# Performance work log

Measured on AMD Instinct MI355X. Metric: run time of the kernel, lower is better.

The kernel has to match this reference:

```python
import jax, jax.numpy as jnp
import numpy as np

NUM_EMBEDDINGS = 8192
EMBEDDING_DIM = 64
COMMITMENT_COST = 0.25


def setup_inputs() -> dict:
    key = jax.random.key(0)
    kx, ke = jax.random.split(key)
    x = jax.random.normal(kx, (32, 1024, EMBEDDING_DIM), dtype=jnp.float32)
    embeddings = jax.random.normal(ke, (NUM_EMBEDDINGS, EMBEDDING_DIM), dtype=jnp.float32)
    return {"x": x, "embeddings": embeddings}


def reference(x, embeddings):
    d = embeddings.shape[1]
    flat_x = x.reshape(-1, d)  # [N, D]
    # squared euclidean distances (argmin identical to cdist argmin):
    d2 = (
        jnp.sum(flat_x * flat_x, axis=-1, keepdims=True)
        - 2.0 * flat_x @ embeddings.T
        + jnp.sum(embeddings * embeddings, axis=-1)
    )
    encoding_indices = jnp.argmin(d2, axis=1)  # [N]
    quantized = embeddings[encoding_indices].reshape(x.shape)
    codebook_loss = jnp.mean((jax.lax.stop_gradient(quantized) - x) ** 2)
    commitment_loss = COMMITMENT_COST * jnp.mean((quantized - jax.lax.stop_gradient(x)) ** 2)
    loss = codebook_loss + commitment_loss
    # straight-through estimator
    quantized_st = x + jax.lax.stop_gradient(quantized - x)
    return quantized_st, loss, encoding_indices
```

## Files before the change

### kernel.cpp

```cpp
#include <hip/hip_runtime.h>
#include <hip/hip_bf16.h>
#include <float.h>

#define N_ROWS 32768
#define DIMS   64
#define K_EMB  8192
#define NT     (K_EMB / 16)
#define NQ     8
#define NTQ    (NT / NQ)
#define TSTAGE 4
#define NSTAGE (NTQ / TSTAGE)
#define RG     4
#define KEYMASK 0xFFFFFFC0u
#define GAP_THR 3.5e-3f

typedef __attribute__((ext_vector_type(8))) short s8v;
typedef __attribute__((ext_vector_type(4))) float f4v;
typedef __attribute__((ext_vector_type(4))) int   i4v;

#define WS_EFRAG 0
#define WS_EN2   (2 * 1024 * 1024)
#define WS_IDX   (WS_EN2 + K_EMB * 4)
#define WS_KEY   (WS_IDX + N_ROWS * 4)
#define WS_BH    (WS_KEY + N_ROWS * 8)
#define WS_SH    (WS_BH + NQ * N_ROWS * 4)
#define WS_CH    (WS_SH + NQ * N_ROWS * 4)
#define WS_CTL   (WS_CH + NQ * N_ROWS * 4)
#define WS_WL    (WS_CTL + 16)

#define OUT_LOSS (N_ROWS * DIMS)
#define OUT_IDX  (N_ROWS * DIMS + 1)

__device__ inline short bfh(float v) {
    __hip_bfloat16 h = __float2bfloat16(v);
    return __builtin_bit_cast(short, h);
}
__device__ inline float bff(short s) {
    __hip_bfloat16 h = __builtin_bit_cast(__hip_bfloat16, s);
    return __bfloat162float(h);
}

__global__ void vq_prep(const float* __restrict__ emb, short* __restrict__ efrag,
                        float* __restrict__ en2, int4* __restrict__ ctl) {
    if (blockIdx.x == 0 && threadIdx.x == 0) *ctl = make_int4(0, 0, 0, 0);
    int gid = blockIdx.x * 256 + threadIdx.x;
    int t = gid >> 6, lane = gid & 63;
    int m = lane & 15, q = lane >> 4;
    const float* er = emb + (size_t)(t * 16 + m) * DIMS;
    s8v hi0, lo0, hi1, lo1;
    float ss = 0.f;
#pragma unroll
    for (int j = 0; j < 8; ++j) {
        float v0 = er[q * 8 + j];
        float v1 = er[32 + q * 8 + j];
        ss += v0 * v0 + v1 * v1;
        short h0 = bfh(v0); lo0[j] = bfh(v0 - bff(h0)); hi0[j] = h0;
        short h1 = bfh(v1); lo1[j] = bfh(v1 - bff(h1)); hi1[j] = h1;
    }
    s8v* base = (s8v*)efrag + (size_t)t * 4 * 64;
    base[0 * 64 + lane] = hi0;
    base[1 * 64 + lane] = hi1;
    base[2 * 64 + lane] = lo0;
    base[3 * 64 + lane] = lo1;
    ss += __shfl_xor(ss, 16, 64);
    ss += __shfl_xor(ss, 32, 64);
    if (q == 0) en2[t * 16 + m] = -0.5f * ss;
}

__global__ __launch_bounds__(256)
__attribute__((amdgpu_waves_per_eu(2, 4))) void vq_phase1(
    const float* __restrict__ x, const short* __restrict__ efrag,
    const float* __restrict__ en2,
    float* __restrict__ bh, float* __restrict__ sh, int* __restrict__ ch) {
    __shared__ __align__(16) char lds[2][TSTAGE * 4096];
    int tid = threadIdx.x, wid = tid >> 6, lane = tid & 63;
    int m = lane & 15, q = lane >> 4;
    int kh = blockIdx.y;
    int row0 = blockIdx.x * 256 + wid * 64;

    s8v ahi[RG][2], alo[RG][2];
#pragma unroll
    for (int g = 0; g < RG; ++g) {
        const float* xr = x + (size_t)(row0 + g * 16 + m) * DIMS + q * 8;
#pragma unroll
        for (int j = 0; j < 8; ++j) {
            float v0 = xr[j], v1 = xr[32 + j];
            short h0 = bfh(v0); alo[g][0][j] = bfh(v0 - bff(h0)); ahi[g][0][j] = h0;
            short h1 = bfh(v1); alo[g][1][j] = bfh(v1 - bff(h1)); ahi[g][1][j] = h1;
        }
    }

    float best[RG][4], sec[RG][4];
#pragma unroll
    for (int g = 0; g < RG; ++g)
#pragma unroll
        for (int r = 0; r < 4; ++r) { best[g][r] = -FLT_MAX; sec[g][r] = -FLT_MAX; }

    const char* gsrc = (const char*)efrag + (size_t)kh * NTQ * 4096;

#pragma unroll
    for (int i = 0; i < TSTAGE; ++i)
        __builtin_amdgcn_global_load_lds(
            (const __attribute__((address_space(1))) void*)(gsrc + i * 4096 + tid * 16),
            (__attribute__((address_space(3))) void*)(&lds[0][i * 4096 + tid * 16]),
            16, 0, 0);
    __syncthreads();

    for (int s = 0; s < NSTAGE; ++s) {
        int pb = s & 1;
        if (s + 1 < NSTAGE) {
            const char* gn = gsrc + (size_t)(s + 1) * TSTAGE * 4096;
#pragma unroll
            for (int i = 0; i < TSTAGE; ++i)
                __builtin_amdgcn_global_load_lds(
                    (const __attribute__((address_space(1))) void*)(gn + i * 4096 + tid * 16),
                    (__attribute__((address_space(3))) void*)(&lds[pb ^ 1][i * 4096 + tid * 16]),
                    16, 0, 0);
        }
        const i4v* B = (const i4v*)(lds[pb]);
        const float* ep = en2 + (size_t)(kh * NTQ + s * TSTAGE) * 16 + m;
#pragma unroll
        for (int tt = 0; tt < TSTAGE; ++tt) {
            i4v b0 = B[tt * 256 + 0 * 64 + lane];
            i4v b1 = B[tt * 256 + 1 * 64 + lane];
            i4v b2 = B[tt * 256 + 2 * 64 + lane];
            i4v b3 = B[tt * 256 + 3 * 64 + lane];
            float c0 = ep[tt * 16];
            unsigned code = (unsigned)(s * TSTAGE + tt);
            f4v cinit = {c0, c0, c0, c0};
#pragma unroll
            for (int g = 0; g < RG; ++g) {
                f4v acc;
                acc = __builtin_amdgcn_mfma_f32_16x16x32_bf16(ahi[g][0], __builtin_bit_cast(s8v, b0), cinit, 0, 0, 0);
                acc = __builtin_amdgcn_mfma_f32_16x16x32_bf16(ahi[g][1], __builtin_bit_cast(s8v, b1), acc, 0, 0, 0);
                acc = __builtin_amdgcn_mfma_f32_16x16x32_bf16(ahi[g][0], __builtin_bit_cast(s8v, b2), acc, 0, 0, 0);
                acc = __builtin_amdgcn_mfma_f32_16x16x32_bf16(ahi[g][1], __builtin_bit_cast(s8v, b3), acc, 0, 0, 0);
                acc = __builtin_amdgcn_mfma_f32_16x16x32_bf16(alo[g][0], __builtin_bit_cast(s8v, b0), acc, 0, 0, 0);
                acc = __builtin_amdgcn_mfma_f32_16x16x32_bf16(alo[g][1], __builtin_bit_cast(s8v, b1), acc, 0, 0, 0);
#pragma unroll
                for (int r = 0; r < 4; ++r) {
                    float kf = __uint_as_float(
                        (__float_as_uint(acc[r]) & KEYMASK) | code);
                    sec[g][r]  = __builtin_amdgcn_fmed3f(kf, sec[g][r], best[g][r]);
                    best[g][r] = fmaxf(best[g][r], kf);
                }
            }
        }
        __syncthreads();
    }

#pragma unroll
    for (int g = 0; g < RG; ++g)
#pragma unroll
    for (int r = 0; r < 4; ++r) {
        float b = best[g][r], sv = sec[g][r];
#pragma unroll
        for (int off = 1; off < 16; off <<= 1) {
            float ob = __shfl_xor(b, off, 64);
            float os = __shfl_xor(sv, off, 64);
            sv = fmaxf(fminf(b, ob), fmaxf(sv, os));
            b  = fmaxf(b, ob);
        }
        unsigned long long bal =
            __ballot(__float_as_uint(best[g][r]) == __float_as_uint(b));
        int win = __ffsll(bal >> (q * 16)) - 1;
        if (m == win) {
            int tl  = (int)(__float_as_uint(b) & 63u);
            int col = ((kh * NTQ + tl) << 4) | m;
            int o = kh * N_ROWS + row0 + g * 16 + q * 4 + r;
            bh[o] = b; sh[o] = sv; ch[o] = col;
        }
    }
}

__global__ void vq_merge(const float* __restrict__ bh, const float* __restrict__ sh,
                         const int* __restrict__ ch, int* __restrict__ idx_buf,
                         unsigned long long* __restrict__ key8,
                         float* __restrict__ nbv,
                         int* __restrict__ wl, int* __restrict__ wl_count) {
    int row = blockIdx.x * 256 + threadIdx.x;
    float nb = bh[row];
    int   c  = ch[row];
    float ns = -FLT_MAX;
#pragma unroll
    for (int h = 1; h < NQ; ++h) {
        float b = bh[h * N_ROWS + row];
        int   cc = ch[h * N_ROWS + row];
        if (b > nb) { ns = nb; nb = b; c = cc; }
        else        { ns = fmaxf(ns, b); }
    }
#pragma unroll
    for (int h = 0; h < NQ; ++h) ns = fmaxf(ns, sh[h * N_ROWS + row]);
    idx_buf[row] = c;
    key8[row] = 0ULL;
    nbv[row] = nb;
    if (nb - ns < GAP_THR) {
        int pos = atomicAdd(wl_count, 1);
        wl[pos] = row;
    }
}

__global__ __launch_bounds__(64) void vq_fixup(
    const float* __restrict__ x, const float* __restrict__ emb,
    const float* __restrict__ en2, const float* __restrict__ nbv,
    unsigned long long* __restrict__ key8,
    const int* __restrict__ wl, const int* __restrict__ wl_count) {
    int lane = threadIdx.x;
    int cchunk = blockIdx.x & 127;
    int rslice = blockIdx.x >> 7;
    int cnt = *wl_count;
    if (rslice >= cnt) return;
    int c = cchunk * 64 + lane;
    const float4* er = (const float4*)(emb + (size_t)c * DIMS);
    float4 e[16];
#pragma unroll
    for (int qq = 0; qq < 16; ++qq) e[qq] = er[qq];
    float c0 = en2[c];
    for (int wi = rslice; wi < cnt; wi += 16) {
        int row = wl[wi];
        const float4* xr = (const float4*)(x + (size_t)row * DIMS);
        float d = 0.f;
#pragma unroll
        for (int qq = 0; qq < 16; ++qq) {
            float4 ee = e[qq];
            float4 xx = xr[qq];
            d += ee.x * xx.x + ee.y * xx.y + ee.z * xx.z + ee.w * xx.w;
        }
        float bf_ = d + c0;
        int bc_ = c;
#pragma unroll
        for (int off = 1; off < 64; off <<= 1) {
            float of = __shfl_xor(bf_, off, 64);
            int   oc = __shfl_xor(bc_, off, 64);
            if (of > bf_ || (of == bf_ && oc < bc_)) { bf_ = of; bc_ = oc; }
        }
        if (lane == 0 && bf_ >= nbv[row] - GAP_THR) {
            unsigned int u = __float_as_uint(bf_);
            unsigned int sb = ((int)u < 0) ? ~u : (u | 0x80000000u);
            unsigned long long key = ((unsigned long long)sb << 32) | (unsigned int)(~bc_);
            atomicMax(&key8[row], key);
        }
    }
}

__global__ void vq_gather(const float* __restrict__ x, const float* __restrict__ emb,
                          const int* __restrict__ idx_buf,
                          const unsigned long long* __restrict__ key8,
                          float* __restrict__ out, double* __restrict__ loss_acc,
                          int* __restrict__ done_count) {
    int row = blockIdx.x * blockDim.x + threadIdx.x;
    unsigned long long k = key8[row];
    int idx = k ? (int)(~(unsigned int)k) : idx_buf[row];
    const float4* ev = (const float4*)(emb + (size_t)idx * DIMS);
    const float4* xv = (const float4*)(x + (size_t)row * DIMS);
    float4* ov = (float4*)(out + (size_t)row * DIMS);
    float s = 0.f;
#pragma unroll
    for (int qq = 0; qq < 16; ++qq) {
        float4 ee = ev[qq];
        float4 xx = xv[qq];
        float dx = ee.x - xx.x, dy = ee.y - xx.y, dz = ee.z - xx.z, dw = ee.w - xx.w;
        s += dx * dx + dy * dy + dz * dz + dw * dw;
        ov[qq] = ee;
    }
#pragma unroll
    for (int off = 32; off > 0; off >>= 1) s += __shfl_down(s, off, 64);
    if ((threadIdx.x & 63) == 0) atomicAdd(loss_acc, (double)s);
    out[OUT_IDX + row] = (float)idx;
    __syncthreads();
    if (threadIdx.x == 0) {
        __threadfence();
        int d = atomicAdd(done_count, 1);
        if (d == (int)gridDim.x - 1) {
            double total = atomicAdd(loss_acc, 0.0);
            out[OUT_LOSS] = (float)(1.25 * total / (double)(N_ROWS * DIMS));
        }
    }
}

extern "C" void kernel_launch(void* const* d_in, const int* in_sizes, int n_in,
                              void* d_out, int out_size, void* d_ws, size_t ws_size,
                              hipStream_t stream) {
    const float* x   = (const float*)d_in[0];
    const float* emb = (const float*)d_in[1];
    float* out = (float*)d_out;
    char*  ws  = (char*)d_ws;

    short* efrag   = (short*)(ws + WS_EFRAG);
    float* en2     = (float*)(ws + WS_EN2);
    int*   idx_buf = (int*)(ws + WS_IDX);
    unsigned long long* key8 = (unsigned long long*)(ws + WS_KEY);
    float* bhb     = (float*)(ws + WS_BH);
    float* shb     = (float*)(ws + WS_SH);
    int*   chb     = (int*)(ws + WS_CH);
    double* loss_acc = (double*)(ws + WS_CTL);
    int*   wl_count  = (int*)(ws + WS_CTL + 8);
    int*   done_cnt  = (int*)(ws + WS_CTL + 12);
    int*   wl        = (int*)(ws + WS_WL);

    vq_prep<<<(NT * 64) / 256, 256, 0, stream>>>(emb, efrag, en2, (int4*)(ws + WS_CTL));
    vq_phase1<<<dim3(N_ROWS / 256, NQ), 256, 0, stream>>>(x, efrag, en2, bhb, shb, chb);
    vq_merge<<<N_ROWS / 256, 256, 0, stream>>>(bhb, shb, chb, idx_buf, key8, bhb, wl, wl_count);
    vq_fixup<<<2048, 64, 0, stream>>>(x, emb, en2, bhb, key8, wl, wl_count);
    vq_gather<<<N_ROWS / 256, 256, 0, stream>>>(x, emb, idx_buf, key8, out, loss_acc, done_cnt);
}
```

Before: 191.3 us.

## Replace LDS-staged codebook pipeline with direct global loads in single-wave blocks

The main distance kernel no longer stages codebook fragments through double-buffered shared memory with block-wide barriers. Each single-wave block now reads B fragments straight from global memory (L2-cached) into registers, using a two-tile software prefetch. This removes LDS traffic and __syncthreads stalls and lets waves run independently. The cost is redundant global/L2 reads per wave (four times more per-wave fetches, since the four waves that used to share one LDS copy now each load their own) and possible exposed load latency. The prep kernel's block size is also halved.

```diff
diff --git a/kernel.cpp b/kernel.cpp
--- a/kernel.cpp
+++ b/kernel.cpp
@@ -8,8 +8,6 @@
 #define NT     (K_EMB / 16)
 #define NQ     8
 #define NTQ    (NT / NQ)
-#define TSTAGE 4
-#define NSTAGE (NTQ / TSTAGE)
 #define RG     4
 #define KEYMASK 0xFFFFFFC0u
 #define GAP_THR 3.5e-3f
@@ -43,7 +41,7 @@
 __global__ void vq_prep(const float* __restrict__ emb, short* __restrict__ efrag,
                         float* __restrict__ en2, int4* __restrict__ ctl) {
     if (blockIdx.x == 0 && threadIdx.x == 0) *ctl = make_int4(0, 0, 0, 0);
-    int gid = blockIdx.x * 256 + threadIdx.x;
+    int gid = blockIdx.x * 128 + threadIdx.x;
     int t = gid >> 6, lane = gid & 63;
     int m = lane & 15, q = lane >> 4;
     const float* er = emb + (size_t)(t * 16 + m) * DIMS;
@@ -67,16 +65,43 @@
     if (q == 0) en2[t * 16 + m] = -0.5f * ss;
 }
 
-__global__ __launch_bounds__(256)
-__attribute__((amdgpu_waves_per_eu(2, 4))) void vq_phase1(
+#define LOADT(B0, B1, B2, B3, CC, T) do {                 \
+    const i4v* _p = bsrc + (size_t)(T) * 256;             \
+    B0 = _p[lane];       B1 = _p[64 + lane];              \
+    B2 = _p[128 + lane]; B3 = _p[192 + lane];             \
+    CC = ep[(T) * 16];                                    \
+} while (0)
+
+#define COMPT(B0, B1, B2, B3, CC, CODE) do {                                     \
+    f4v cinit = {CC, CC, CC, CC};                 \
+    _Pragma("unroll")                                                            \
+    for (int g = 0; g < RG; ++g) {                                               \
+        f4v acc;                                                                 \
+        acc = __builtin_amdgcn_mfma_f32_16x16x32_bf16(ahi[g][0], __builtin_bit_cast(s8v, B0), cinit, 0, 0, 0); \
+        acc = __builtin_amdgcn_mfma_f32_16x16x32_bf16(ahi[g][1], __builtin_bit_cast(s8v, B1), acc, 0, 0, 0);   \
+        acc = __builtin_amdgcn_mfma_f32_16x16x32_bf16(ahi[g][0], __builtin_bit_cast(s8v, B2), acc, 0, 0, 0);   \
+        acc = __builtin_amdgcn_mfma_f32_16x16x32_bf16(ahi[g][1], __builtin_bit_cast(s8v, B3), acc, 0, 0, 0);   \
+        acc = __builtin_amdgcn_mfma_f32_16x16x32_bf16(alo[g][0], __builtin_bit_cast(s8v, B0), acc, 0, 0, 0);   \
+        acc = __builtin_amdgcn_mfma_f32_16x16x32_bf16(alo[g][1], __builtin_bit_cast(s8v, B1), acc, 0, 0, 0);   \
+        _Pragma("unroll")                                                        \
+        for (int r = 0; r < 4; ++r) {        \
+            float kf = __uint_as_float(                                          \
+                (__float_as_uint(acc[r]) & KEYMASK) | (unsigned)(CODE));         \
+            sec[g][r]  = __builtin_amdgcn_fmed3f(kf, sec[g][r], best[g][r]);     \
+            best[g][r] = fmaxf(best[g][r], kf);                                  \
+        }                                                                        \
+    }                                                                            \
+} while (0)
+
+__global__ __launch_bounds__(64)
+__attribute__((amdgpu_waves_per_eu(2, 3))) void vq_phase1(
     const float* __restrict__ x, const short* __restrict__ efrag,
     const float* __restrict__ en2,
     float* __restrict__ bh, float* __restrict__ sh, int* __restrict__ ch) {
-    __shared__ __align__(16) char lds[2][TSTAGE * 4096];
-    int tid = threadIdx.x, wid = tid >> 6, lane = tid & 63;
+    int lane = threadIdx.x;
     int m = lane & 15, q = lane >> 4;
     int kh = blockIdx.y;
-    int row0 = blockIdx.x * 256 + wid * 64;
+    int row0 = blockIdx.x * 64;
 
     s8v ahi[RG][2], alo[RG][2];
 #pragma unroll
@@ -96,57 +121,18 @@
 #pragma unroll
         for (int r = 0; r < 4; ++r) { best[g][r] = -FLT_MAX; sec[g][r] = -FLT_MAX; }
 
-    const char* gsrc = (const char*)efrag + (size_t)kh * NTQ * 4096;
-
-#pragma unroll
-    for (int i = 0; i < TSTAGE; ++i)
-        __builtin_amdgcn_global_load_lds(
-            (const __attribute__((address_space(1))) void*)(gsrc + i * 4096 + tid * 16),
-            (__attribute__((address_space(3))) void*)(&lds[0][i * 4096 + tid * 16]),
-            16, 0, 0);
-    __syncthreads();
-
-    for (int s = 0; s < NSTAGE; ++s) {
-        int pb = s & 1;
-        if (s + 1 < NSTAGE) {
-            const char* gn = gsrc + (size_t)(s + 1) * TSTAGE * 4096;
-#pragma unroll
-            for (int i = 0; i < TSTAGE; ++i)
-                __builtin_amdgcn_global_load_lds(
-                    (const __attribute__((address_space(1))) void*)(gn + i * 4096 + tid * 16),
-                    (__attribute__((address_space(3))) void*)(&lds[pb ^ 1][i * 4096 + tid * 16]),
-                    16, 0, 0);
-        }
-        const i4v* B = (const i4v*)(lds[pb]);
-        const float* ep = en2 + (size_t)(kh * NTQ + s * TSTAGE) * 16 + m;
-#pragma unroll
-        for (int tt = 0; tt < TSTAGE; ++tt) {
-            i4v b0 = B[tt * 256 + 0 * 64 + lane];
-            i4v b1 = B[tt * 256 + 1 * 64 + lane];
-            i4v b2 = B[tt * 256 + 2 * 64 + lane];
-            i4v b3 = B[tt * 256 + 3 * 64 + lane];
-            float c0 = ep[tt * 16];
-            unsigned code = (unsigned)(s * TSTAGE + tt);
-            f4v cinit = {c0, c0, c0, c0};
-#pragma unroll
-            for (int g = 0; g < RG; ++g) {
-                f4v acc;
-                acc = __builtin_amdgcn_mfma_f32_16x16x32_bf16(ahi[g][0], __builtin_bit_cast(s8v, b0), cinit, 0, 0, 0);
-                acc = __builtin_amdgcn_mfma_f32_16x16x32_bf16(ahi[g][1], __builtin_bit_cast(s8v, b1), acc, 0, 0, 0);
-                acc = __builtin_amdgcn_mfma_f32_16x16x32_bf16(ahi[g][0], __builtin_bit_cast(s8v, b2), acc, 0, 0, 0);
-                acc = __builtin_amdgcn_mfma_f32_16x16x32_bf16(ahi[g][1], __builtin_bit_cast(s8v, b3), acc, 0, 0, 0);
-                acc = __builtin_amdgcn_mfma_f32_16x16x32_bf16(alo[g][0], __builtin_bit_cast(s8v, b0), acc, 0, 0, 0);
-                acc = __builtin_amdgcn_mfma_f32_16x16x32_bf16(alo[g][1], __builtin_bit_cast(s8v, b1), acc, 0, 0, 0);
-#pragma unroll
-                for (int r = 0; r < 4; ++r) {
-                    float kf = __uint_as_float(
-                        (__float_as_uint(acc[r]) & KEYMASK) | code);
-                    sec[g][r]  = __builtin_amdgcn_fmed3f(kf, sec[g][r], best[g][r]);
-                    best[g][r] = fmaxf(best[g][r], kf);
-                }
-            }
-        }
-        __syncthreads();
+    const i4v*   bsrc = (const i4v*)efrag + (size_t)kh * NTQ * 256;
+    const float* ep   = en2 + (size_t)kh * NTQ * 16 + m;
+
+    i4v A0, A1, A2, A3, B0, B1, B2, B3;
+    float cA, cB;
+    LOADT(A0, A1, A2, A3, cA, 0);
+#pragma unroll 1
+    for (int t = 0; t < NTQ; t += 2) {
+        LOADT(B0, B1, B2, B3, cB, t + 1);
+        COMPT(A0, A1, A2, A3, cA, t);
+        if (t + 2 < NTQ) LOADT(A0, A1, A2, A3, cA, t + 2);
+        COMPT(B0, B1, B2, B3, cB, t + 1);
     }
 
 #pragma unroll
@@ -298,8 +284,8 @@
     int*   done_cnt  = (int*)(ws + WS_CTL + 12);
     int*   wl        = (int*)(ws + WS_WL);
 
-    vq_prep<<<(NT * 64) / 256, 256, 0, stream>>>(emb, efrag, en2, (int4*)(ws + WS_CTL));
-    vq_phase1<<<dim3(N_ROWS / 256, NQ), 256, 0, stream>>>(x, efrag, en2, bhb, shb, chb);
+    vq_prep<<<(NT * 64) / 128, 128, 0, stream>>>(emb, efrag, en2, (int4*)(ws + WS_CTL));
+    vq_phase1<<<dim3(N_ROWS / 64, NQ), 64, 0, stream>>>(x, efrag, en2, bhb, shb, chb);
     vq_merge<<<N_ROWS / 256, 256, 0, stream>>>(bhb, shb, chb, idx_buf, key8, bhb, wl, wl_count);
     vq_fixup<<<2048, 64, 0, stream>>>(x, emb, en2, bhb, key8, wl, wl_count);
     vq_gather<<<N_ROWS / 256, 256, 0, stream>>>(x, emb, idx_buf, key8, out, loss_acc, done_cnt);
```

Result: no change. 193.4 us (+1.1%).
